# Performance work log

Measured on AMD Instinct MI355X. Metric: run time of the kernel, lower is better.

## Reference

```python
import jax, jax.numpy as jnp
import numpy as np

HEADS = 4
DIM_K = 16
DIM_U = 1
EPS = 1e-5


def _rel_pos_idx(n):
    # torch: meshgrid(ij) -> stack -> '(i j) n'; rel = pos[None,:]-pos[:,None] + n-1
    ii, jj = np.meshgrid(np.arange(n), np.arange(n), indexing='ij')
    pos = np.stack([ii, jj]).reshape(2, -1).T  # (n*n, 2)
    rel = pos[None, :] - pos[:, None] + (n - 1)  # (N, N, 2)
    return rel[..., 0], rel[..., 1]


def _bn(t, gamma, beta):
    # BatchNorm2d in training mode: batch stats over (b, h, w), biased var
    mu = t.mean(axis=(0, 1, 2))
    var = t.var(axis=(0, 1, 2))
    return (t - mu) * jax.lax.rsqrt(var + EPS) * gamma + beta


def setup_inputs() -> dict:
    key = jax.random.key(0)
    ks = jax.random.split(key, 16)
    b, n, c = 8, 48, 128
    hk = DIM_K * HEADS          # 64
    v = 128 // HEADS            # 32 (dim_out // heads)
    rl = 2 * n - 1              # 95
    s = 0.02
    return {
        'x': jax.random.normal(ks[0], (b, n, n, c), jnp.float32),
        'cor': jax.random.normal(ks[1], (b, n, n, 2), jnp.float32),
        'Wq': jax.random.normal(ks[2], (hk, c), jnp.float32) * s,
        'Wk': jax.random.normal(ks[3], (DIM_K * DIM_U, c), jnp.float32) * s,
        'Wv': jax.random.normal(ks[4], (v * DIM_U, c), jnp.float32) * s,
        'Wce': jax.random.normal(ks[5], (hk, 2), jnp.float32) * s,
        'bce': jax.random.normal(ks[6], (hk,), jnp.float32) * s,
        'Wcc': jax.random.normal(ks[7], (hk, 128), jnp.float32) * s,
        'Wmp': jax.random.normal(ks[8], (128, hk), jnp.float32) * s,
        'bmp': jax.random.normal(ks[9], (128,), jnp.float32) * s,
        'gq': jnp.ones((hk,), jnp.float32),
        'bq': jnp.zeros((hk,), jnp.float32),
        'gv': jnp.ones((v * DIM_U,), jnp.float32),
        'bv': jnp.zeros((v * DIM_U,), jnp.float32),
        'rel_pos_emb': jax.random.normal(ks[10], (rl, rl, DIM_K, DIM_U), jnp.float32),
    }


def reference(x, cor, Wq, Wk, Wv, Wce, bce, Wcc, Wmp, bmp, gq, bq, gv, bv, rel_pos_emb):
    b, hh, ww, c = x.shape
    h, u, kd = HEADS, DIM_U, DIM_K
    vd = Wv.shape[0] // u
    N = hh * ww

    # frame reversal along batch
    x_rev = jnp.concatenate([x[b // 2:], x[:b // 2]], axis=0)

    # 1x1 convs as channel matmuls (channels-last)
    q = jnp.einsum('bhwc,oc->bhwo', x, Wq)
    k = jnp.einsum('bhwc,oc->bhwo', x_rev, Wk)
    v = jnp.einsum('bhwc,oc->bhwo', x_rev, Wv)

    Qn = _bn(q, gq, bq)
    Vn = _bn(v, gv, bv)

    Q = jnp.transpose(Qn.reshape(b, N, h, kd), (0, 2, 3, 1))       # b h k n
    K = jnp.transpose(k.reshape(b, N, u, kd), (0, 2, 3, 1))        # b u k m
    V = jnp.transpose(Vn.reshape(b, N, u, vd), (0, 2, 3, 1))       # b u v m

    K = jax.nn.softmax(K, axis=-1)
    lamc = jnp.einsum('bukm,buvm->bkv', K, V)
    Yc = jnp.einsum('bhkn,bkv->bhvn', Q, lamc)

    # relative position lambda (global branch)
    ni, mi = _rel_pos_idx(hh)
    emb = rel_pos_emb[ni, mi]                                      # n m k u
    lamp = jnp.einsum('nmku,buvm->bnkv', emb, V)
    Yp = jnp.einsum('bhkn,bnkv->bhvn', Q, lamp)

    Y = Yc + Yp                                                    # b h v n
    appearance = jnp.transpose(Y.reshape(b, h, vd, hh, ww), (0, 3, 4, 1, 2)).reshape(b, hh, ww, h * vd)

    cor_embed_ = jnp.einsum('bhwc,oc->bhwo', cor, Wce) + bce       # b hh ww (h k)
    cor_embed = jnp.transpose(cor_embed_.reshape(b, N, h, kd), (0, 2, 3, 1))  # b h k n
    crc = jnp.einsum('bhkn,bkv->bhvn', cor_embed, lamc)
    crp = jnp.einsum('bhkn,bnkv->bhvn', cor_embed, lamp)
    cor_reverse_ = jnp.transpose((crc + crp).reshape(b, h, vd, hh, ww), (0, 3, 4, 1, 2)).reshape(b, hh, ww, h * vd)
    cor_reverse = jnp.einsum('bhwc,oc->bhwo', cor_reverse_, Wcc)
    motion = jnp.einsum('bhwc,oc->bhwo', cor_reverse - cor_embed_, Wmp) + bmp
    return appearance, motion
```

## Files before the change

kernel.cpp:

```cpp
#include <hip/hip_runtime.h>
#include <math.h>
#include <stdint.h>

#define NNPOS 2304
#define ROWS  18432
#define NK    96

#define O_Q   0ul
#define O_K   1179648ul
#define O_V   1474560ul
#define O_ST  2064384ul
#define O_VP  2064704ul
#define O_QP  2457920ul
#define O_LC  4817216ul
#define O_CR  4821312ul
#define O_RT  6000960ul
#define O_WG  6148416ul
#define O_B2  6148672ul
#define O_WB  6148800ul
#define O_PT  6155968ul
#define O_PV  6164160ul
#define O_PE  6166208ul
#define O_WFB 6167232ul

typedef __bf16 bf16x8 __attribute__((ext_vector_type(8)));
typedef float  f32x4  __attribute__((ext_vector_type(4)));
typedef unsigned int u32;
typedef u32 u32x4 __attribute__((ext_vector_type(4)));

__device__ __forceinline__ void gll16(const void* g, void* l) {
  auto gp = (const __attribute__((address_space(1))) unsigned char*)(uintptr_t)g;
  auto lp = (__attribute__((address_space(3))) unsigned char*)(u32)(uintptr_t)l;
  __builtin_amdgcn_global_load_lds(gp, lp, 16, 0, 0);
}

__global__ void k_fold(const float* __restrict__ Wcc, const float* __restrict__ Wce,
                       const float* __restrict__ Wmp, const float* __restrict__ bmp,
                       const float* __restrict__ bce, const float* __restrict__ Wq,
                       const float* __restrict__ Wk, const float* __restrict__ Wv,
                       float* __restrict__ ws) {
  const int t = threadIdx.x;
  const int g = blockIdx.x * 256 + t;
  const int o2 = g >> 7, c = g & 127;
  float acc = 0.f;
#pragma unroll 8
  for (int o = 0; o < 64; ++o) acc += Wmp[o2 * 64 + o] * Wcc[o * 128 + c];
  ((__bf16*)(ws + O_WFB))[o2 * 128 + c] = (__bf16)acc;
  if (blockIdx.x == 0 && t < 128) {
    float a0 = 0.f, a1 = 0.f, ab = 0.f;
#pragma unroll 8
    for (int o = 0; o < 64; ++o) {
      float w = Wmp[t * 64 + o];
      a0 += w * Wce[o * 2]; a1 += w * Wce[o * 2 + 1]; ab += w * bce[o];
    }
    ws[O_WG + t * 2] = a0; ws[O_WG + t * 2 + 1] = a1; ws[O_B2 + t] = bmp[t] - ab;
  }
  __bf16* wbp = (__bf16*)(ws + O_WB);
  if (g < 14336) {
    float w;
    if (g < 8192) w = Wq[g];
    else if (g < 10240) w = Wk[g - 8192];
    else w = Wv[g - 10240];
    wbp[g] = (__bf16)w;
  }
}

__global__ __launch_bounds__(256) void k_qkv(const float* __restrict__ x,
                                             float* __restrict__ ws) {
  const int t = threadIdx.x;
  const int wave = t >> 6, lane = t & 63;
  const int lr = lane & 15, quad = lane >> 4;
  const int r0 = blockIdx.x * 64 + wave * 16;
  const int b = r0 / NNPOS;
  const int n0 = r0 - b * NNPOS;
  const size_t outbase = (size_t)(((b + 4) & 7)) * NNPOS + n0;

  const __bf16* wb = (const __bf16*)(ws + O_WB);
  const float* xrow = x + (size_t)(r0 + lr) * 128;

  f32x4 acc[7];
#pragma unroll
  for (int i = 0; i < 7; ++i) acc[i] = (f32x4){0.f, 0.f, 0.f, 0.f};

#pragma unroll
  for (int ks = 0; ks < 4; ++ks) {
    const float* ap = xrow + ks * 32 + quad * 8;
    float4 a0 = *(const float4*)(ap);
    float4 a1 = *(const float4*)(ap + 4);
    bf16x8 af;
    af[0] = (__bf16)a0.x; af[1] = (__bf16)a0.y; af[2] = (__bf16)a0.z; af[3] = (__bf16)a0.w;
    af[4] = (__bf16)a1.x; af[5] = (__bf16)a1.y; af[6] = (__bf16)a1.z; af[7] = (__bf16)a1.w;
#pragma unroll
    for (int ct = 0; ct < 7; ++ct) {
      bf16x8 bfrag = *(const bf16x8*)(wb + (ct * 16 + lr) * 128 + ks * 32 + quad * 8);
      acc[ct] = __builtin_amdgcn_mfma_f32_16x16x32_bf16(af, bfrag, acc[ct], 0, 0, 0);
    }
  }

#pragma unroll
  for (int ct = 0; ct < 7; ++ct) {
#pragma unroll
    for (int reg = 0; reg < 4; ++reg) {
      int m = quad * 4 + reg;
      int oc = ct * 16 + lr;
      float vvv = acc[ct][reg];
      if (ct < 4)      ws[O_Q + (size_t)(r0 + m) * 64 + oc] = vvv;
      else if (ct < 5) ws[O_K + (outbase + m) * 16 + (oc - 64)] = vvv;
      else             ws[O_V + (outbase + m) * 32 + (oc - 80)] = vvv;
    }
  }
}

__global__ void k_rt(const float* __restrict__ rel, float* __restrict__ ws) {
  __bf16* rt = (__bf16*)(ws + O_RT);
  int i = blockIdx.x * 256 + threadIdx.x;
  if (i < 144400) {
    int kc = i & 15, rr = i >> 4;
    int ri = rr / 95, rj = rr - ri * 95;
    rt[(size_t)kc * 9216 + ri * 96 + rj] = (__bf16)rel[i];
  }
}

__global__ void k_zero(float* __restrict__ ws) {
  __bf16* vp = (__bf16*)(ws + O_VP);
  int i = blockIdx.x * 256 + threadIdx.x;
  if (i < 4096) ws[O_LC + i] = 0.f;
  int bv = i / 96, rem = i - bv * 96;
  int mi = rem >> 1, h8 = rem & 1;
  uint4 z; z.x = 0; z.y = 0; z.z = 0; z.w = 0;
  *(uint4*)(vp + (size_t)bv * 3072 + mi * 64 + 48 + h8 * 8) = z;
}

__global__ void k_stats1(float* __restrict__ ws) {
  const int t = threadIdx.x, blk = blockIdx.x;
  __shared__ float sh[512];
  if (blk < 64) {
    const int ch = t & 63, rsub = t >> 6;
    const float* src = ws + O_Q;
    const int r0 = blk * 288;
    float s = 0.f, s2 = 0.f;
#pragma unroll 4
    for (int i = 0; i < 72; ++i) {
      float v = src[(size_t)(r0 + rsub + i * 4) * 64 + ch];
      s += v; s2 += v * v;
    }
    sh[t] = s; sh[256 + t] = s2;
    __syncthreads();
    if (t < 64) {
      float S = sh[t] + sh[t + 64] + sh[t + 128] + sh[t + 192];
      float S2 = sh[256 + t] + sh[256 + t + 64] + sh[256 + t + 128] + sh[256 + t + 192];
      ws[O_PT + blk * 128 + t * 2] = S; ws[O_PT + blk * 128 + t * 2 + 1] = S2;
    }
  } else if (blk < 96) {
    const int j = blk - 64;
    const int ch = t & 31, rsub = t >> 5;
    const float* src = ws + O_V;
    const int r0 = j * 576;
    float s = 0.f, s2 = 0.f;
#pragma unroll 4
    for (int i = 0; i < 72; ++i) {
      float v = src[(size_t)(r0 + rsub + i * 8) * 32 + ch];
      s += v; s2 += v * v;
    }
    sh[t] = s; sh[256 + t] = s2;
    __syncthreads();
    if (t < 32) {
      float S = 0.f, S2 = 0.f;
#pragma unroll
      for (int k = 0; k < 8; ++k) { S += sh[t + k * 32]; S2 += sh[256 + t + k * 32]; }
      ws[O_PV + j * 64 + t * 2] = S; ws[O_PV + j * 64 + t * 2 + 1] = S2;
    }
  } else {
    const int idx = blk - 96;
    const int b = idx >> 3, sl = idx & 7;
    const int kc = t & 15, rsub = t >> 4;
    const int r0 = b * 2304 + sl * 288;
    float s = 0.f;
#pragma unroll 2
    for (int i = 0; i < 18; ++i)
      s += __expf(ws[O_K + (size_t)(r0 + rsub + i * 16) * 16 + kc]);
    sh[t] = s;
    __syncthreads();
    if (t < 16) {
      float S = 0.f;
#pragma unroll
      for (int k = 0; k < 16; ++k) S += sh[t + k * 16];
      ws[O_PE + b * 128 + sl * 16 + t] = S;
    }
  }
}

__global__ void k_stats2(const float* __restrict__ gq, const float* __restrict__ bq,
                         const float* __restrict__ gv, const float* __restrict__ bv,
                         float* __restrict__ ws) {
  const int t = threadIdx.x;
  if (t < 64) {
    float S = 0.f, S2 = 0.f;
    for (int i = 0; i < 64; ++i) { S += ws[O_PT + i * 128 + t * 2]; S2 += ws[O_PT + i * 128 + t * 2 + 1]; }
    float mu = S / 18432.f, var = S2 / 18432.f - mu * mu;
    float sc = gq[t] * rsqrtf(var + 1e-5f);
    ws[O_ST + t] = sc; ws[O_ST + 64 + t] = bq[t] - mu * sc;
  } else if (t < 96) {
    int ch = t - 64;
    float S = 0.f, S2 = 0.f;
    for (int i = 0; i < 32; ++i) { S += ws[O_PV + i * 64 + ch * 2]; S2 += ws[O_PV + i * 64 + ch * 2 + 1]; }
    float mu = S / 18432.f, var = S2 / 18432.f - mu * mu;
    float sc = gv[ch] * rsqrtf(var + 1e-5f);
    ws[O_ST + 128 + ch] = sc; ws[O_ST + 160 + ch] = bv[ch] - mu * sc;
  } else if (t < 224) {
    int idx = t - 96; int b = idx >> 4, kc = idx & 15;
    float S = 0.f;
#pragma unroll
    for (int sl = 0; sl < 8; ++sl) S += ws[O_PE + b * 128 + sl * 16 + kc];
    ws[O_ST + 192 + idx] = 1.f / S;
  }
}

__global__ void k_vp(float* __restrict__ ws) {
  const int b = blockIdx.x / 48, mi = blockIdx.x - b * 48;
  const int t = threadIdx.x;
  __shared__ float Vn[48 * 33];
  const float* st = ws + O_ST;
  const int r0 = b * 2304 + mi * 48;
#pragma unroll
  for (int i = t; i < 1536; i += 256) {
    int r = i >> 5, j = i & 31;
    Vn[r * 33 + j] = ws[O_V + (size_t)(r0 + r) * 32 + j] * st[128 + j] + st[160 + j];
  }
  __syncthreads();
  __bf16* vp = (__bf16*)(ws + O_VP);
  const int j = t >> 3, seg = t & 7;
  unsigned short u[6];
#pragma unroll
  for (int q = 0; q < 6; ++q)
    u[q] = __builtin_bit_cast(unsigned short, (__bf16)Vn[(seg * 6 + q) * 33 + j]);
  u32 w0 = (u32)u[0] | ((u32)u[1] << 16);
  u32 w1 = (u32)u[2] | ((u32)u[3] << 16);
  u32 w2 = (u32)u[4] | ((u32)u[5] << 16);
  u32* dst = (u32*)(vp + (size_t)(b * 32 + j) * 3072 + mi * 64 + seg * 6);
  dst[0] = w0; dst[1] = w1; dst[2] = w2;
}

__global__ void k_prep(const float* __restrict__ cor, const float* __restrict__ Wce,
                       const float* __restrict__ bce, float* __restrict__ ws) {
  const int t = threadIdx.x;
  const int rl = t >> 5, j = t & 31;
  const int rid = blockIdx.x * 8 + rl;
  const int b = rid / NNPOS, n = rid - b * NNPOS;
  const float* st = ws + O_ST;
  float c0 = cor[rid * 2], c1 = cor[rid * 2 + 1];
#pragma unroll
  for (int ch = j; ch < 64; ch += 32) {
    float qn = ws[O_Q + (size_t)rid * 64 + ch] * st[ch] + st[64 + ch];
    ws[O_QP + (size_t)(n * 8 + b) * 128 + ch] = qn;
    float ce = c0 * Wce[ch * 2] + c1 * Wce[ch * 2 + 1] + bce[ch];
    ws[O_QP + (size_t)(n * 8 + b) * 128 + 64 + ch] = ce;
  }
}

__global__ void k_lamc(float* __restrict__ ws) {
  const int b = blockIdx.x / 36, sl = blockIdx.x - b * 36;
  const int t = threadIdx.x;
  __shared__ float eK[16][16];
  __shared__ float Vn[16][33];
  const float* st = ws + O_ST;
  const int kc = t & 15, vp_ = t >> 4;
  const int v0 = vp_ * 2, v1 = v0 + 1;
  float a0 = 0.f, a1 = 0.f;
  const int m0 = b * 2304 + sl * 64;
  const int jj = t & 31, rw = t >> 5;
  const float scj = st[128 + jj], bij = st[160 + jj];
  for (int ch = 0; ch < 4; ++ch) {
    const int mbase = m0 + ch * 16;
    eK[t >> 4][t & 15] = __expf(ws[O_K + (size_t)(mbase + (t >> 4)) * 16 + (t & 15)]);
    Vn[rw][jj]     = ws[O_V + (size_t)(mbase + rw) * 32 + jj] * scj + bij;
    Vn[rw + 8][jj] = ws[O_V + (size_t)(mbase + rw + 8) * 32 + jj] * scj + bij;
    __syncthreads();
#pragma unroll
    for (int m = 0; m < 16; ++m) {
      float e = eK[m][kc];
      a0 += e * Vn[m][v0];
      a1 += e * Vn[m][v1];
    }
    __syncthreads();
  }
  atomicAdd(&ws[O_LC + (size_t)(b * 16 + kc) * 32 + v0], a0);
  atomicAdd(&ws[O_LC + (size_t)(b * 16 + kc) * 32 + v1], a1);
}

__global__ __launch_bounds__(256, 2) void k_lamp(float* __restrict__ ws,
                                                 float* __restrict__ out) {
  __shared__ __align__(16) char smem[33792];
  bf16x8* Bs16 = (bf16x8*)smem;
  u32* Sw = (u32*)(smem + 16384);
  float* Cs = (float*)smem;

  const int t = threadIdx.x;
  const int bx = blockIdx.x;
  const int ni = bx / 6;
  const int sset = bx - ni * 6;
  const int s0 = (sset < 3) ? sset * 16 : (sset - 3) * 16 + 1;
  const int chalf = blockIdx.y;
  const int colbase = chalf * 128;
  const int w = t >> 6, lane = t & 63;
  const int wrow = w >> 1, wcol = w & 1;
  const int lr = lane & 15, quad = lane >> 4;

  const __bf16* vp = (const __bf16*)(ws + O_VP);
  const unsigned short* rp = (const unsigned short*)(ws + O_RT);

  const int kcA0 = t / 24, wpA0 = t - kcA0 * 24;
  const int ia1 = t + 256;
  const int kcA1 = ia1 / 24, wpA1 = ia1 - kcA1 * 24;
  const bool hasA1 = (t < 128);

  const int u0 = w * 64 + lane, u1 = 256 + w * 64 + lane;
  const int cB0 = u0 >> 2, pB0 = ((u0 & 3) - ((u0 >> 3) & 3)) & 3;
  const int cB1 = u1 >> 2, pB1 = ((u1 & 3) - ((u1 >> 3) & 3)) & 3;
  const __bf16* gB0 = vp + (size_t)(colbase + cB0) * 3072 + pB0 * 8;
  const __bf16* gB1 = vp + (size_t)(colbase + cB1) * 3072 + pB1 * 8;
  char* ldsB0 = smem + w * 1024;
  char* ldsB1 = smem + 4096 + w * 1024;

  auto gatherA = [&](int ksn, u32& a0_, u32& a1_) {
    const int mi = ksn >> 1, mj0 = (ksn & 1) << 5;
    const int P0 = 96 * (mi - ni + 47) + mj0 - s0 + 33;
    long b0 = (long)kcA0 * 9216 + P0 + 2 * wpA0;
    if (P0 & 1) a0_ = (u32)rp[b0] | ((u32)rp[b0 + 1] << 16);
    else        a0_ = *(const u32*)(rp + b0);
    if (hasA1) {
      long b1 = (long)kcA1 * 9216 + P0 + 2 * wpA1;
      if (P0 & 1) a1_ = (u32)rp[b1] | ((u32)rp[b1 + 1] << 16);
      else        a1_ = *(const u32*)(rp + b1);
    }
  };

  f32x4 acc[4][4];
  {
    f32x4 zz = {0.f, 0.f, 0.f, 0.f};
#pragma unroll
    for (int i = 0; i < 4; ++i)
#pragma unroll
      for (int j = 0; j < 4; ++j) acc[i][j] = zz;
  }

  u32 a0 = 0, a1 = 0;
  {
    u32 p0, p1 = 0;
    gatherA(0, p0, p1);
    Sw[kcA0 * 25 + wpA0] = p0;
    if (hasA1) Sw[kcA1 * 25 + wpA1] = p1;
    gll16(gB0, ldsB0);
    gll16(gB1, ldsB1);
    gatherA(1, a0, a1);
  }
  __syncthreads();

  for (int ks = 0; ks < NK; ++ks) {
    const int cur = ks & 1, nxt = cur ^ 1;
    if (ks + 1 < NK) {
      const int k0n = (ks + 1) * 32;
      gll16(gB0 + k0n, ldsB0 + nxt * 8192);
      gll16(gB1 + k0n, ldsB1 + nxt * 8192);
      Sw[nxt * 400 + kcA0 * 25 + wpA0] = a0;
      if (hasA1) Sw[nxt * 400 + kcA1 * 25 + wpA1] = a1;
    }
    if (ks + 2 < NK) gatherA(ks + 2, a0, a1);

    bf16x8 af[4], bfr[4];
#pragma unroll
    for (int rt = 0; rt < 4; ++rt) {
      int nl = wrow * 4 + rt;
      int wb = cur * 400 + lr * 25 + (7 - nl) + quad * 4;
      u32x4 dd = { Sw[wb], Sw[wb + 1], Sw[wb + 2], Sw[wb + 3] };
      af[rt] = __builtin_bit_cast(bf16x8, dd);
    }
#pragma unroll
    for (int ct = 0; ct < 4; ++ct) {
      int col = wcol * 64 + ct * 16 + lr;
      bfr[ct] = Bs16[cur * 512 + col * 4 + ((quad + (col >> 1)) & 3)];
    }
#pragma unroll
    for (int rt = 0; rt < 4; ++rt)
#pragma unroll
      for (int ct = 0; ct < 4; ++ct)
        acc[rt][ct] = __builtin_amdgcn_mfma_f32_16x16x32_bf16(af[rt], bfr[ct], acc[rt][ct], 0, 0, 0);
    __syncthreads();
  }

  const float* lamcp = ws + O_LC;
  const float* Qp = ws + O_QP;
  __bf16* CRb = (__bf16*)(ws + O_CR);
  const int s = t >> 5, vv = t & 31;

  for (int h = 0; h < 2; ++h) {
    __syncthreads();
    if (wrow == h) {
#pragma unroll
      for (int rt = 0; rt < 4; ++rt) {
#pragma unroll
        for (int ct = 0; ct < 4; ++ct) {
          int col = wcol * 64 + ct * 16 + lr;
          int bb = chalf * 4 + (col >> 5);
          int vl = col & 31;
#pragma unroll
          for (int reg = 0; reg < 4; ++reg) {
            int row = rt * 16 + quad * 4 + reg;
            int kc = row & 15;
            float dinv = ws[O_ST + 192 + bb * 16 + kc];
            Cs[row * 132 + col] = acc[rt][ct][reg] + lamcp[(bb * 16 + kc) * 32 + vl] * dinv;
          }
        }
      }
    }
    __syncthreads();
#pragma unroll
    for (int i = 0; i < 16; ++i) {
      int combo = s * 16 + i;
      int hp = combo & 7, bl = (combo >> 3) & 3, nr = combo >> 5;
      int n = ni * 48 + s0 + 2 * (h * 4 + nr);
      int bb = chalf * 4 + bl;
      const float* qrow = Qp + ((size_t)(n * 8 + bb) * 8 + hp) * 16;
      const float* crow = Cs + (nr * 16) * 132 + bl * 32 + vv;
      float y = 0.f;
#pragma unroll
      for (int kc = 0; kc < 16; ++kc) y += qrow[kc] * crow[kc * 132];
      size_t idx = (size_t)(bb * NNPOS + n) * 128 + (hp & 3) * 32 + vv;
      if (hp < 4) out[idx] = y;
      else        CRb[idx] = (__bf16)y;
    }
  }
}

__global__ __launch_bounds__(256) void k_motion(const float* __restrict__ cor,
                                                float* __restrict__ ws,
                                                float* __restrict__ out) {
  const int t = threadIdx.x;
  const int wave = t >> 6, lane = t & 63;
  const int lr = lane & 15, quad = lane >> 4;
  const int r0 = blockIdx.x * 64 + wave * 16;
  const __bf16* crb = (const __bf16*)(ws + O_CR);
  const __bf16* wfb = (const __bf16*)(ws + O_WFB);

  f32x4 acc[8];
#pragma unroll
  for (int i = 0; i < 8; ++i) acc[i] = (f32x4){0.f, 0.f, 0.f, 0.f};

#pragma unroll
  for (int ks = 0; ks < 4; ++ks) {
    bf16x8 af = *(const bf16x8*)(crb + (size_t)(r0 + lr) * 128 + ks * 32 + quad * 8);
#pragma unroll
    for (int ct = 0; ct < 8; ++ct) {
      bf16x8 bfrag = *(const bf16x8*)(wfb + (ct * 16 + lr) * 128 + ks * 32 + quad * 8);
      acc[ct] = __builtin_amdgcn_mfma_f32_16x16x32_bf16(af, bfrag, acc[ct], 0, 0, 0);
    }
  }

#pragma unroll
  for (int reg = 0; reg < 4; ++reg) {
    int row = r0 + quad * 4 + reg;
    float c0 = cor[row * 2], c1 = cor[row * 2 + 1];
#pragma unroll
    for (int ct = 0; ct < 8; ++ct) {
      int o2 = ct * 16 + lr;
      float y = acc[ct][reg] + ws[O_B2 + o2] - c0 * ws[O_WG + o2 * 2] - c1 * ws[O_WG + o2 * 2 + 1];
      out[2359296ul + (size_t)row * 128 + o2] = y;
    }
  }
}

extern "C" void kernel_launch(void* const* d_in, const int* in_sizes, int n_in,
                              void* d_out, int out_size, void* d_ws, size_t ws_size,
                              hipStream_t stream) {
  const float* x   = (const float*)d_in[0];
  const float* cor = (const float*)d_in[1];
  const float* Wq  = (const float*)d_in[2];
  const float* Wk  = (const float*)d_in[3];
  const float* Wv  = (const float*)d_in[4];
  const float* Wce = (const float*)d_in[5];
  const float* bce = (const float*)d_in[6];
  const float* Wcc = (const float*)d_in[7];
  const float* Wmp = (const float*)d_in[8];
  const float* bmp = (const float*)d_in[9];
  const float* gq  = (const float*)d_in[10];
  const float* bq  = (const float*)d_in[11];
  const float* gv  = (const float*)d_in[12];
  const float* bv  = (const float*)d_in[13];
  const float* rel = (const float*)d_in[14];
  float* out = (float*)d_out;
  float* ws  = (float*)d_ws;

  k_fold  <<<64, 256, 0, stream>>>(Wcc, Wce, Wmp, bmp, bce, Wq, Wk, Wv, ws);
  k_qkv   <<<288, 256, 0, stream>>>(x, ws);
  k_rt    <<<565, 256, 0, stream>>>(rel, ws);
  k_zero  <<<96, 256, 0, stream>>>(ws);
  k_stats1<<<160, 256, 0, stream>>>(ws);
  k_stats2<<<1, 256, 0, stream>>>(gq, bq, gv, bv, ws);
  k_vp    <<<384, 256, 0, stream>>>(ws);
  k_lamc  <<<288, 256, 0, stream>>>(ws);
  k_prep  <<<2304, 256, 0, stream>>>(cor, Wce, bce, ws);
  k_lamp  <<<dim3(288, 2), 256, 0, stream>>>(ws, out);
  k_motion<<<288, 256, 0, stream>>>(cor, ws, out);
}
```

Baseline: 268.0 us.

## Split lamp K loop across two blocks with atomic accumulation into zeroed outputs

Adds a third grid dimension so each k_lamp block handles half of the 96 K steps, doubling the block count from 576 to 1152. Partial results go into the appearance output and a new fp32 cor-reverse buffer through atomicAdd, both cleared by a new k_zout kernel. The double-buffered global_load_lds pipeline is replaced by a simpler register-staged single buffer with two syncs per step. The cost is extra zeroing traffic, fp32 atomics, and an fp32 intermediate in place of bf16, in exchange for better occupancy of the GPU's compute units.

```diff
diff --git a/kernel.cpp b/kernel.cpp
--- a/kernel.cpp
+++ b/kernel.cpp
@@ -13,7 +13,6 @@
 #define O_VP  2064704ul
 #define O_QP  2457920ul
 #define O_LC  4817216ul
-#define O_CR  4821312ul
 #define O_RT  6000960ul
 #define O_WG  6148416ul
 #define O_B2  6148672ul
@@ -22,17 +21,12 @@
 #define O_PV  6164160ul
 #define O_PE  6166208ul
 #define O_WFB 6167232ul
+#define O_CRF 6175424ul
 
 typedef __bf16 bf16x8 __attribute__((ext_vector_type(8)));
 typedef float  f32x4  __attribute__((ext_vector_type(4)));
 typedef unsigned int u32;
 typedef u32 u32x4 __attribute__((ext_vector_type(4)));
-
-__device__ __forceinline__ void gll16(const void* g, void* l) {
-  auto gp = (const __attribute__((address_space(1))) unsigned char*)(uintptr_t)g;
-  auto lp = (__attribute__((address_space(3))) unsigned char*)(u32)(uintptr_t)l;
-  __builtin_amdgcn_global_load_lds(gp, lp, 16, 0, 0);
-}
 
 __global__ void k_fold(const float* __restrict__ Wcc, const float* __restrict__ Wce,
                        const float* __restrict__ Wmp, const float* __restrict__ bmp,
@@ -129,6 +123,13 @@
   int mi = rem >> 1, h8 = rem & 1;
   uint4 z; z.x = 0; z.y = 0; z.z = 0; z.w = 0;
   *(uint4*)(vp + (size_t)bv * 3072 + mi * 64 + 48 + h8 * 8) = z;
+}
+
+__global__ void k_zout(float* __restrict__ out, float* __restrict__ ws) {
+  size_t i = (size_t)blockIdx.x * 256 + threadIdx.x;
+  f32x4 z = {0.f, 0.f, 0.f, 0.f};
+  ((f32x4*)out)[i] = z;
+  ((f32x4*)(ws + O_CRF))[i] = z;
 }
 
 __global__ void k_stats1(float* __restrict__ ws) {
@@ -292,7 +293,7 @@
                                                  float* __restrict__ out) {
   __shared__ __align__(16) char smem[33792];
   bf16x8* Bs16 = (bf16x8*)smem;
-  u32* Sw = (u32*)(smem + 16384);
+  u32* Sw = (u32*)(smem + 8192);
   float* Cs = (float*)smem;
 
   const int t = threadIdx.x;
@@ -301,39 +302,27 @@
   const int sset = bx - ni * 6;
   const int s0 = (sset < 3) ? sset * 16 : (sset - 3) * 16 + 1;
   const int chalf = blockIdx.y;
+  const int khalf = blockIdx.z;
+  const int ks0 = khalf * 48, ksE = ks0 + 48;
   const int colbase = chalf * 128;
-  const int w = t >> 6, lane = t & 63;
-  const int wrow = w >> 1, wcol = w & 1;
+  const int wave = t >> 6, lane = t & 63;
+  const int wrow = wave >> 1, wcol = wave & 1;
   const int lr = lane & 15, quad = lane >> 4;
 
   const __bf16* vp = (const __bf16*)(ws + O_VP);
   const unsigned short* rp = (const unsigned short*)(ws + O_RT);
 
-  const int kcA0 = t / 24, wpA0 = t - kcA0 * 24;
+  const int ia0 = t;
+  const int kcA0 = ia0 / 24, wpA0 = ia0 - kcA0 * 24;
   const int ia1 = t + 256;
   const int kcA1 = ia1 / 24, wpA1 = ia1 - kcA1 * 24;
-  const bool hasA1 = (t < 128);
-
-  const int u0 = w * 64 + lane, u1 = 256 + w * 64 + lane;
-  const int cB0 = u0 >> 2, pB0 = ((u0 & 3) - ((u0 >> 3) & 3)) & 3;
-  const int cB1 = u1 >> 2, pB1 = ((u1 & 3) - ((u1 >> 3) & 3)) & 3;
-  const __bf16* gB0 = vp + (size_t)(colbase + cB0) * 3072 + pB0 * 8;
-  const __bf16* gB1 = vp + (size_t)(colbase + cB1) * 3072 + pB1 * 8;
-  char* ldsB0 = smem + w * 1024;
-  char* ldsB1 = smem + 4096 + w * 1024;
-
-  auto gatherA = [&](int ksn, u32& a0_, u32& a1_) {
-    const int mi = ksn >> 1, mj0 = (ksn & 1) << 5;
-    const int P0 = 96 * (mi - ni + 47) + mj0 - s0 + 33;
-    long b0 = (long)kcA0 * 9216 + P0 + 2 * wpA0;
-    if (P0 & 1) a0_ = (u32)rp[b0] | ((u32)rp[b0 + 1] << 16);
-    else        a0_ = *(const u32*)(rp + b0);
-    if (hasA1) {
-      long b1 = (long)kcA1 * 9216 + P0 + 2 * wpA1;
-      if (P0 & 1) a1_ = (u32)rp[b1] | ((u32)rp[b1 + 1] << 16);
-      else        a1_ = *(const u32*)(rp + b1);
-    }
-  };
+  const bool hasA1 = (ia1 < 384);
+
+  const int colB0 = t >> 2, pB0 = ((t & 3) - ((t >> 3) & 3)) & 3;
+  const int ub1 = t + 256;
+  const int colB1 = ub1 >> 2, pB1 = ((ub1 & 3) - ((ub1 >> 3) & 3)) & 3;
+  const __bf16* gB0 = vp + (size_t)(colbase + colB0) * 3072 + pB0 * 8;
+  const __bf16* gB1 = vp + (size_t)(colbase + colB1) * 3072 + pB1 * 8;
 
   f32x4 acc[4][4];
   {
@@ -344,53 +333,61 @@
       for (int j = 0; j < 4; ++j) acc[i][j] = zz;
   }
 
-  u32 a0 = 0, a1 = 0;
-  {
-    u32 p0, p1 = 0;
-    gatherA(0, p0, p1);
-    Sw[kcA0 * 25 + wpA0] = p0;
-    if (hasA1) Sw[kcA1 * 25 + wpA1] = p1;
-    gll16(gB0, ldsB0);
-    gll16(gB1, ldsB1);
-    gatherA(1, a0, a1);
-  }
-  __syncthreads();
-
-  for (int ks = 0; ks < NK; ++ks) {
-    const int cur = ks & 1, nxt = cur ^ 1;
-    if (ks + 1 < NK) {
-      const int k0n = (ks + 1) * 32;
-      gll16(gB0 + k0n, ldsB0 + nxt * 8192);
-      gll16(gB1 + k0n, ldsB1 + nxt * 8192);
-      Sw[nxt * 400 + kcA0 * 25 + wpA0] = a0;
-      if (hasA1) Sw[nxt * 400 + kcA1 * 25 + wpA1] = a1;
-    }
-    if (ks + 2 < NK) gatherA(ks + 2, a0, a1);
+  u32 sa0 = 0, sa1 = 0;
+  bf16x8 vb0, vb1;
+
+  auto loadStep = [&](int ksn) {
+    const int mi = ksn >> 1, mj0 = (ksn & 1) << 5;
+    const int P0 = 96 * (mi - ni + 47) + mj0 - s0 + 33;
+    const int k0 = ksn * 32;
+    long b0 = (long)kcA0 * 9216 + P0 + 2 * wpA0;
+    if (P0 & 1) sa0 = (u32)rp[b0] | ((u32)rp[b0 + 1] << 16);
+    else        sa0 = *(const u32*)(rp + b0);
+    if (hasA1) {
+      long b1 = (long)kcA1 * 9216 + P0 + 2 * wpA1;
+      if (P0 & 1) sa1 = (u32)rp[b1] | ((u32)rp[b1 + 1] << 16);
+      else        sa1 = *(const u32*)(rp + b1);
+    }
+    vb0 = *(const bf16x8*)(gB0 + k0);
+    vb1 = *(const bf16x8*)(gB1 + k0);
+  };
+
+  loadStep(ks0);
+
+  for (int ks = ks0; ks < ksE; ++ks) {
+    __syncthreads();
+    Sw[kcA0 * 25 + wpA0] = sa0;
+    if (hasA1) Sw[kcA1 * 25 + wpA1] = sa1;
+    Bs16[t] = vb0;
+    Bs16[t + 256] = vb1;
+    __syncthreads();
+
+    if (ks + 1 < ksE) loadStep(ks + 1);
 
     bf16x8 af[4], bfr[4];
 #pragma unroll
     for (int rt = 0; rt < 4; ++rt) {
       int nl = wrow * 4 + rt;
-      int wb = cur * 400 + lr * 25 + (7 - nl) + quad * 4;
+      int wb = lr * 25 + (7 - nl) + quad * 4;
       u32x4 dd = { Sw[wb], Sw[wb + 1], Sw[wb + 2], Sw[wb + 3] };
       af[rt] = __builtin_bit_cast(bf16x8, dd);
     }
 #pragma unroll
     for (int ct = 0; ct < 4; ++ct) {
       int col = wcol * 64 + ct * 16 + lr;
-      bfr[ct] = Bs16[cur * 512 + col * 4 + ((quad + (col >> 1)) & 3)];
+      int u = col * 4 + ((quad + (col >> 1)) & 3);
+      bfr[ct] = Bs16[u];
     }
 #pragma unroll
     for (int rt = 0; rt < 4; ++rt)
 #pragma unroll
       for (int ct = 0; ct < 4; ++ct)
         acc[rt][ct] = __builtin_amdgcn_mfma_f32_16x16x32_bf16(af[rt], bfr[ct], acc[rt][ct], 0, 0, 0);
-    __syncthreads();
   }
 
   const float* lamcp = ws + O_LC;
   const float* Qp = ws + O_QP;
-  __bf16* CRb = (__bf16*)(ws + O_CR);
+  float* crf = ws + O_CRF;
   const int s = t >> 5, vv = t & 31;
 
   for (int h = 0; h < 2; ++h) {
@@ -407,8 +404,12 @@
           for (int reg = 0; reg < 4; ++reg) {
             int row = rt * 16 + quad * 4 + reg;
             int kc = row & 15;
-            float dinv = ws[O_ST + 192 + bb * 16 + kc];
-            Cs[row * 132 + col] = acc[rt][ct][reg] + lamcp[(bb * 16 + kc) * 32 + vl] * dinv;
+            float add = 0.f;
+            if (khalf == 0) {
+              float dinv = ws[O_ST + 192 + bb * 16 + kc];
+              add = lamcp[(bb * 16 + kc) * 32 + vl] * dinv;
+            }
+            Cs[row * 132 + col] = acc[rt][ct][reg] + add;
           }
         }
       }
@@ -426,8 +427,8 @@
 #pragma unroll
       for (int kc = 0; kc < 16; ++kc) y += qrow[kc] * crow[kc * 132];
       size_t idx = (size_t)(bb * NNPOS + n) * 128 + (hp & 3) * 32 + vv;
-      if (hp < 4) out[idx] = y;
-      else        CRb[idx] = (__bf16)y;
+      if (hp < 4) atomicAdd(&out[idx], y);
+      else        atomicAdd(&crf[idx], y);
     }
   }
 }
@@ -439,7 +440,7 @@
   const int wave = t >> 6, lane = t & 63;
   const int lr = lane & 15, quad = lane >> 4;
   const int r0 = blockIdx.x * 64 + wave * 16;
-  const __bf16* crb = (const __bf16*)(ws + O_CR);
+  const float* crf = ws + O_CRF;
   const __bf16* wfb = (const __bf16*)(ws + O_WFB);
 
   f32x4 acc[8];
@@ -448,7 +449,12 @@
 
 #pragma unroll
   for (int ks = 0; ks < 4; ++ks) {
-    bf16x8 af = *(const bf16x8*)(crb + (size_t)(r0 + lr) * 128 + ks * 32 + quad * 8);
+    const float* ap = crf + (size_t)(r0 + lr) * 128 + ks * 32 + quad * 8;
+    float4 a0 = *(const float4*)(ap);
+    float4 a1 = *(const float4*)(ap + 4);
+    bf16x8 af;
+    af[0] = (__bf16)a0.x; af[1] = (__bf16)a0.y; af[2] = (__bf16)a0.z; af[3] = (__bf16)a0.w;
+    af[4] = (__bf16)a1.x; af[5] = (__bf16)a1.y; af[6] = (__bf16)a1.z; af[7] = (__bf16)a1.w;
 #pragma unroll
     for (int ct = 0; ct < 8; ++ct) {
       bf16x8 bfrag = *(const bf16x8*)(wfb + (ct * 16 + lr) * 128 + ks * 32 + quad * 8);
@@ -494,11 +500,12 @@
   k_qkv   <<<288, 256, 0, stream>>>(x, ws);
   k_rt    <<<565, 256, 0, stream>>>(rel, ws);
   k_zero  <<<96, 256, 0, stream>>>(ws);
+  k_zout  <<<2304, 256, 0, stream>>>(out, ws);
   k_stats1<<<160, 256, 0, stream>>>(ws);
   k_stats2<<<1, 256, 0, stream>>>(gq, bq, gv, bv, ws);
   k_vp    <<<384, 256, 0, stream>>>(ws);
   k_lamc  <<<288, 256, 0, stream>>>(ws);
   k_prep  <<<2304, 256, 0, stream>>>(cor, Wce, bce, ws);
-  k_lamp  <<<dim3(288, 2), 256, 0, stream>>>(ws, out);
+  k_lamp  <<<dim3(288, 2, 2), 256, 0, stream>>>(ws, out);
   k_motion<<<288, 256, 0, stream>>>(cor, ws, out);
 }
```

Measured after the change: 252.8 us. 5.7% less time.
